# Kernel optimization log

Hardware: AMD Instinct MI355X
Metric: run time of the kernel (lower is better)

## Reference

```python
import jax, jax.numpy as jnp
import numpy as np

N_U = 50000
N_I = 50000
E = 800000
HID = 64
HEADS = 4
OUT = 32
NEG_SLOPE = 0.2


def _gat(xs, xd, e, ws, wd, a_s, a_d, b, heads, ch, n_dst, concat):
    # xs:[Ns,Fin] xd:[Nd,Fin] e:[2,E]; PyG GATConv (no self loops, eval mode)
    hs = (xs @ ws).reshape(-1, heads, ch)  # [Ns,H,C]
    hd = (xd @ wd).reshape(-1, heads, ch)  # [Nd,H,C]
    al_s = jnp.einsum('nhc,hc->nh', hs, a_s)  # [Ns,H]
    al_d = jnp.einsum('nhc,hc->nh', hd, a_d)  # [Nd,H]
    src, dst = e[0], e[1]
    alpha = jax.nn.leaky_relu(al_s[src] + al_d[dst], NEG_SLOPE)  # [E,H]
    m = jax.lax.stop_gradient(jax.ops.segment_max(alpha, dst, num_segments=n_dst))
    ealpha = jnp.exp(alpha - m[dst])
    denom = jax.ops.segment_sum(ealpha, dst, num_segments=n_dst)
    coef = ealpha / (denom[dst] + 1e-16)  # segment softmax over incoming edges
    msg = hs[src] * coef[:, :, None]  # [E,H,C]
    out = jax.ops.segment_sum(msg, dst, num_segments=n_dst)  # [Nd,H,C]
    out = out.reshape(n_dst, heads * ch) if concat else out.mean(axis=1)
    return out + b


def _forward(x_user, x_item, e_u2i, e_i2u,
             p_user_w, p_user_b, p_item_w, p_item_b,
             l0_u2i_ws, l0_u2i_wd, l0_u2i_as, l0_u2i_ad, l0_u2i_b,
             l0_i2u_ws, l0_i2u_wd, l0_i2u_as, l0_i2u_ad, l0_i2u_b,
             l1_u2i_ws, l1_u2i_wd, l1_u2i_as, l1_u2i_ad, l1_u2i_b,
             l1_i2u_ws, l1_i2u_wd, l1_i2u_as, l1_i2u_ad, l1_i2u_b):
    hu = jax.nn.elu(x_user @ p_user_w + p_user_b)
    hi = jax.nn.elu(x_item @ p_item_w + p_item_b)
    # layer 0: heads=4, concat=True, out dim HID*HEADS; HeteroConv sum (one edge type per dst)
    hi1 = _gat(hu, hi, e_u2i, l0_u2i_ws, l0_u2i_wd, l0_u2i_as, l0_u2i_ad, l0_u2i_b, HEADS, HID, N_I, True)
    hu1 = _gat(hi, hu, e_i2u, l0_i2u_ws, l0_i2u_wd, l0_i2u_as, l0_i2u_ad, l0_i2u_b, HEADS, HID, N_U, True)
    hu1 = jax.nn.elu(hu1)  # dropout is identity in eval mode
    hi1 = jax.nn.elu(hi1)
    # layer 1: heads=1, concat=False -> mean over heads
    hi2 = _gat(hu1, hi1, e_u2i, l1_u2i_ws, l1_u2i_wd, l1_u2i_as, l1_u2i_ad, l1_u2i_b, 1, OUT, N_I, False)
    hu2 = _gat(hi1, hu1, e_i2u, l1_i2u_ws, l1_i2u_wd, l1_i2u_as, l1_i2u_ad, l1_i2u_b, 1, OUT, N_U, False)
    return hu2, hi2


def setup_inputs() -> dict:
    key = jax.random.key(0)
    ks = jax.random.split(key, 32)
    s = 0.1
    d = {
        'x_user': jax.random.normal(ks[0], (N_U, 128), jnp.float32),
        'x_item': jax.random.normal(ks[1], (N_I, 128), jnp.float32),
        'e_u2i': jax.random.randint(ks[2], (2, E), 0, 50000, jnp.int32),
        'e_i2u': jax.random.randint(ks[3], (2, E), 0, 50000, jnp.int32),
        'p_user_w': jax.random.normal(ks[4], (128, HID), jnp.float32) * s,
        'p_user_b': jax.random.normal(ks[5], (HID,), jnp.float32) * s,
        'p_item_w': jax.random.normal(ks[6], (128, HID), jnp.float32) * s,
        'p_item_b': jax.random.normal(ks[7], (HID,), jnp.float32) * s,
    }
    i = 8
    for lname, fin, h, c in (('l0', HID, HEADS, HID), ('l1', HID * HEADS, 1, OUT)):
        for et in ('u2i', 'i2u'):
            odim = h * c if lname == 'l0' else c
            d[f'{lname}_{et}_ws'] = jax.random.normal(ks[i], (fin, h * c), jnp.float32) * s; i += 1
            d[f'{lname}_{et}_wd'] = jax.random.normal(ks[i], (fin, h * c), jnp.float32) * s; i += 1
            d[f'{lname}_{et}_as'] = jax.random.normal(ks[i], (h, c), jnp.float32) * s; i += 1
            d[f'{lname}_{et}_ad'] = jax.random.normal(ks[i], (h, c), jnp.float32) * s; i += 1
            d[f'{lname}_{et}_b'] = jax.random.normal(ks[i], (odim,), jnp.float32) * s; i += 1
    return d


def reference(x_user, x_item, e_u2i, e_i2u,
              p_user_w, p_user_b, p_item_w, p_item_b,
              l0_u2i_ws, l0_u2i_wd, l0_u2i_as, l0_u2i_ad, l0_u2i_b,
              l0_i2u_ws, l0_i2u_wd, l0_i2u_as, l0_i2u_ad, l0_i2u_b,
              l1_u2i_ws, l1_u2i_wd, l1_u2i_as, l1_u2i_ad, l1_u2i_b,
              l1_i2u_ws, l1_i2u_wd, l1_i2u_as, l1_i2u_ad, l1_i2u_b):
    return _forward(x_user, x_item, e_u2i, e_i2u,
                    p_user_w, p_user_b, p_item_w, p_item_b,
                    l0_u2i_ws, l0_u2i_wd, l0_u2i_as, l0_u2i_ad, l0_u2i_b,
                    l0_i2u_ws, l0_i2u_wd, l0_i2u_as, l0_i2u_ad, l0_i2u_b,
                    l1_u2i_ws, l1_u2i_wd, l1_u2i_as, l1_u2i_ad, l1_u2i_b,
                    l1_i2u_ws, l1_i2u_wd, l1_i2u_as, l1_i2u_ad, l1_i2u_b)
```

## Files before the change

### kernel.cpp

```cpp
#include <hip/hip_runtime.h>
#include <cstdint>
#include <cstddef>

#define NN 50000
#define NE 800000
#define GB 196
#define TILE1 4096
#define CAP 8192

typedef __attribute__((ext_vector_type(8))) short short8;
typedef __attribute__((ext_vector_type(4))) float floatx4;

__device__ __forceinline__ float lrelu_f(float x){ return x >= 0.f ? x : 0.2f*x; }
__device__ __forceinline__ float elu_f(float x){ return x > 0.f ? x : __expf(x) - 1.f; }

__device__ __forceinline__ unsigned short f2bf(float f){
  unsigned int u = __float_as_uint(f);
  u += 0x7FFFu + ((u >> 16) & 1u);
  return (unsigned short)(u >> 16);
}
__device__ __forceinline__ float bf2f(unsigned int us){
  return __uint_as_float(us << 16);
}
__device__ __forceinline__ float4 bf4_load(const unsigned short* p){
  uint2 q = *(const uint2*)p;
  return make_float4(bf2f(q.x & 0xffffu), bf2f(q.x >> 16),
                     bf2f(q.y & 0xffffu), bf2f(q.y >> 16));
}
__device__ __forceinline__ uint2 bf4_pack(float4 o){
  uint2 p;
  p.x = (unsigned)f2bf(o.x) | ((unsigned)f2bf(o.y) << 16);
  p.y = (unsigned)f2bf(o.z) | ((unsigned)f2bf(o.w) << 16);
  return p;
}
__device__ __forceinline__ void split_bf(float a, unsigned short& h, unsigned short& l){
  h = f2bf(a);
  l = f2bf(a - bf2f(h));
}

__device__ __forceinline__ float dot2bf(float acc, unsigned a, unsigned b){
  asm("v_dot2_f32_bf16 %0, %1, %2, %0" : "+v"(acc) : "v"(a), "v"(b));
  return acc;
}

__device__ __forceinline__ void agg_pair(float (&acc)[4][8], float (&den)[4],
                                         uint4 q0, uint4 q1, uint2 w0, uint2 w1){
  const unsigned ONE2 = 0x3F803F80u;
  unsigned wp[4];
  wp[0] = __builtin_amdgcn_perm(w1.x, w0.x, 0x05040100u);
  wp[1] = __builtin_amdgcn_perm(w1.x, w0.x, 0x07060302u);
  wp[2] = __builtin_amdgcn_perm(w1.y, w0.y, 0x05040100u);
  wp[3] = __builtin_amdgcn_perm(w1.y, w0.y, 0x07060302u);
  unsigned xp[8];
  xp[0] = __builtin_amdgcn_perm(q1.x, q0.x, 0x05040100u);
  xp[1] = __builtin_amdgcn_perm(q1.x, q0.x, 0x07060302u);
  xp[2] = __builtin_amdgcn_perm(q1.y, q0.y, 0x05040100u);
  xp[3] = __builtin_amdgcn_perm(q1.y, q0.y, 0x07060302u);
  xp[4] = __builtin_amdgcn_perm(q1.z, q0.z, 0x05040100u);
  xp[5] = __builtin_amdgcn_perm(q1.z, q0.z, 0x07060302u);
  xp[6] = __builtin_amdgcn_perm(q1.w, q0.w, 0x05040100u);
  xp[7] = __builtin_amdgcn_perm(q1.w, q0.w, 0x07060302u);
  #pragma unroll
  for (int h=0;h<4;h++){
    den[h] = dot2bf(den[h], wp[h], ONE2);
    #pragma unroll
    for (int c=0;c<8;c++) acc[h][c] = dot2bf(acc[h][c], wp[h], xp[c]);
  }
}

__global__ __launch_bounds__(256) void ghist_kernel(const int* __restrict__ e0,
                                                    const int* __restrict__ e1,
                                                    int* __restrict__ ghist){
  const int ty = blockIdx.y;
  const int* e = ty ? e1 : e0;
  __shared__ int h[GB];
  for (int j=threadIdx.x; j<GB; j+=256) h[j]=0;
  __syncthreads();
  for (int i = blockIdx.x*256 + threadIdx.x; i < NE; i += 256*256)
    atomicAdd(&h[e[NE+i]>>8], 1);
  __syncthreads();
  for (int j=threadIdx.x; j<GB; j+=256) if (h[j]) atomicAdd(&ghist[ty*200+j], h[j]);
}

__global__ __launch_bounds__(256) void gscan_kernel(const int* __restrict__ ghist,
                                                    int* __restrict__ gbase,
                                                    int* __restrict__ gcur){
  __shared__ int wb[4];
  const int t = threadIdx.x, wv = t>>6, l = t&63;
  for (int ty=0; ty<2; ++ty){
    int v = (t < GB) ? ghist[ty*200+t] : 0;
    int sum = v;
    #pragma unroll
    for (int off=1; off<64; off<<=1){
      int x = __shfl_up(sum, off, 64);
      if (l >= off) sum += x;
    }
    if (l == 63) wb[wv] = sum;
    __syncthreads();
    int wbase = 0;
    #pragma unroll
    for (int w=0; w<4; ++w) if (w < wv) wbase += wb[w];
    int excl = wbase + sum - v;
    if (t <= GB) gbase[ty*200+t] = excl;
    if (t <  GB) gcur [ty*200+t] = excl;
    __syncthreads();
  }
}

__global__ __launch_bounds__(256) void part1_kernel(const int* __restrict__ e0,
                                                    const int* __restrict__ e1,
                                                    int* __restrict__ gcur,
                                                    int2* __restrict__ p0,
                                                    int2* __restrict__ p1){
  const int ty = blockIdx.y;
  const int* e = ty ? e1 : e0;
  int2* pairs = ty ? p1 : p0;
  __shared__ int cnt[256];
  __shared__ int lstart[256];
  __shared__ int lcur[256];
  __shared__ int curg[GB];
  __shared__ int lsrc[TILE1];
  __shared__ int ldst[TILE1];
  __shared__ int wb[4];
  const int t = threadIdx.x;
  cnt[t] = 0;
  __syncthreads();
  int dreg[16], sreg[16];
  const int base = blockIdx.x*TILE1;
  const int ntile = min(TILE1, NE - base);
  #pragma unroll
  for (int it=0; it<16; ++it){
    int i = base + it*256 + t;
    int d = -1, s = 0;
    if (i < NE){ d = e[NE+i]; s = e[i]; atomicAdd(&cnt[d>>8], 1); }
    dreg[it] = d; sreg[it] = s;
  }
  __syncthreads();
  int c = cnt[t], sum = c;
  #pragma unroll
  for (int off=1; off<64; off<<=1){
    int x = __shfl_up(sum, off, 64);
    if ((t&63) >= off) sum += x;
  }
  if ((t&63) == 63) wb[t>>6] = sum;
  __syncthreads();
  int wbase = 0;
  #pragma unroll
  for (int w=0; w<4; ++w) if (w < (t>>6)) wbase += wb[w];
  int excl = wbase + sum - c;
  lstart[t] = excl;
  lcur[t] = excl;
  if (t < GB && c > 0) curg[t] = atomicAdd(&gcur[ty*200+t], c);
  __syncthreads();
  #pragma unroll
  for (int it=0; it<16; ++it){
    int d = dreg[it];
    if (d >= 0){
      int pos = atomicAdd(&lcur[d>>8], 1);
      lsrc[pos] = sreg[it];
      ldst[pos] = d;
    }
  }
  __syncthreads();
  for (int i=t; i<ntile; i+=256){
    int d = ldst[i];
    int j = d>>8;
    pairs[curg[j] + (i - lstart[j])] = make_int2(lsrc[i], d);
  }
}

struct Part2Job {
  const int2* pairs; const int* gbase;
  const float* als; const float* ald;
  int* ssrc; int* offs; unsigned short* coef;
};
__global__ __launch_bounds__(256) void part2_kernel(Part2Job j0, Part2Job j1){
  const Part2Job jb = blockIdx.y ? j1 : j0;
  const int b = blockIdx.x;
  const int t = threadIdx.x;
  __shared__ int lcnt[256];
  __shared__ int lcur[256];
  __shared__ int wb[4];
  __shared__ int sorted_src[CAP];
  __shared__ unsigned char sorted_dl[CAP];
  const int gb0 = jb.gbase[b], gb1 = jb.gbase[b+1];
  const int n = gb1 - gb0;
  lcnt[t] = 0;
  __syncthreads();
  for (int i=t; i<n; i+=256)
    atomicAdd(&lcnt[jb.pairs[gb0+i].y - (b<<8)], 1);
  __syncthreads();
  int c = lcnt[t], sum = c;
  #pragma unroll
  for (int off=1; off<64; off<<=1){
    int x = __shfl_up(sum, off, 64);
    if ((t&63) >= off) sum += x;
  }
  if ((t&63) == 63) wb[t>>6] = sum;
  __syncthreads();
  int wbase = 0;
  #pragma unroll
  for (int w=0; w<4; ++w) if (w < (t>>6)) wbase += wb[w];
  int excl = wbase + sum - c;
  lcur[t] = excl;
  int g = (b<<8) + t;
  if (g <= NN) jb.offs[g] = gb0 + excl;
  __syncthreads();
  for (int i=t; i<n; i+=256){
    int2 pr = jb.pairs[gb0+i];
    int dl = pr.y - (b<<8);
    int pos = atomicAdd(&lcur[dl], 1);
    sorted_src[pos] = pr.x;
    sorted_dl[pos] = (unsigned char)dl;
  }
  __syncthreads();
  const float4* als4 = (const float4*)jb.als;
  const float4* ald4 = (const float4*)jb.ald;
  for (int i=t; i<n; i+=256){
    int s  = sorted_src[i];
    int dl = sorted_dl[i];
    float4 a  = als4[s];
    float4 ad = ald4[(b<<8)+dl];
    float4 w;
    w.x = __expf(lrelu_f(a.x+ad.x));
    w.y = __expf(lrelu_f(a.y+ad.y));
    w.z = __expf(lrelu_f(a.z+ad.z));
    w.w = __expf(lrelu_f(a.w+ad.w));
    ((uint2*)jb.coef)[gb0+i] = bf4_pack(w);
    jb.ssrc[gb0+i] = s;
  }
}

struct WcvJob {
  const float* W; const float* cwS; const float* cwD;
  unsigned short* Wth; unsigned short* Wtl;
  int K; int N; int mode;
};
struct WcvArgs { WcvJob j[6]; };
__global__ __launch_bounds__(256) void wconv_kernel(WcvArgs args){
  WcvJob jb = args.j[blockIdx.y];
  int idx = blockIdx.x*256 + threadIdx.x;
  if (idx >= jb.K * jb.N) return;
  int k = idx / jb.N, n = idx % jb.N;
  float val;
  if (jb.mode == 0) val = jb.W[(size_t)k*jb.N + n];
  else {
    if (n < 32)       val = jb.W[(size_t)k*32 + n];
    else if (n == 32) val = jb.cwS[k];
    else if (n == 33) val = jb.cwD[k];
    else              val = 0.f;
  }
  unsigned short h, g;
  split_bf(val, h, g);
  jb.Wth[(size_t)n*jb.K + k] = h;
  jb.Wtl[(size_t)n*jb.K + k] = g;
}

struct MgJob {
  const void* A;
  const unsigned short* Wth;
  const unsigned short* Wtl;
  const float* bias;
  void* C; float* outA; float* outB;
  const float* cwS; const float* cwD;
};
template<int NT, int KK, bool ELU, bool BF16OUT, bool BF16A, bool LG, bool LOGIT>
__global__ __launch_bounds__(256) void mgemm_kernel(MgJob j0, MgJob j1,
                                                    int M, int N)
{
  const MgJob jb = blockIdx.z ? j1 : j0;
  constexpr int TN = NT*16;
  __shared__ __align__(16) unsigned short Ah[64*72];
  __shared__ __align__(16) unsigned short Al[BF16A ? 8 : 64*72];
  __shared__ __align__(16) unsigned short Bh[TN*72];
  __shared__ __align__(16) unsigned short Bl[TN*72];
  __shared__ float CwS[LOGIT ? 256 : 1];
  __shared__ float CwD[LOGIT ? 256 : 1];
  const int t = threadIdx.x;
  const int m0 = blockIdx.x*64;
  const int n0 = blockIdx.y*TN;
  const int wv = t>>6, l = t&63;
  const int lr = l&15, lq = l>>4;
  if constexpr (LOGIT){ CwS[t] = jb.cwS[t]; CwD[t] = jb.cwD[t]; }
  floatx4 acc[NT];
  #pragma unroll
  for (int i=0;i<NT;i++) acc[i] = (floatx4){0.f,0.f,0.f,0.f};

  #pragma unroll
  for (int kt=0; kt<KK; kt+=64){
    if constexpr (BF16A){
      const unsigned short* A = (const unsigned short*)jb.A;
      #pragma unroll
      for (int i=0;i<2;i++){
        int li = t + i*256;
        int r = li >> 3, c8 = (li & 7)*8;
        short8 v = {0,0,0,0,0,0,0,0};
        if (m0 + r < M) v = *(const short8*)(A + (size_t)(m0+r)*KK + kt + c8);
        *(short8*)&Ah[r*72 + c8] = v;
      }
    } else {
      const float* A = (const float*)jb.A;
      #pragma unroll
      for (int i=0;i<4;i++){
        int li = t + i*256;
        int r = li >> 4, c4 = (li & 15)*4;
        float4 v = make_float4(0.f,0.f,0.f,0.f);
        if (m0 + r < M) v = *(const float4*)(A + (size_t)(m0+r)*KK + kt + c4);
        unsigned short h0,h1,h2,h3,g0,g1,g2,g3;
        split_bf(v.x,h0,g0); split_bf(v.y,h1,g1);
        split_bf(v.z,h2,g2); split_bf(v.w,h3,g3);
        uint2 ph = { (unsigned)h0 | ((unsigned)h1<<16), (unsigned)h2 | ((unsigned)h3<<16) };
        uint2 pl = { (unsigned)g0 | ((unsigned)g1<<16), (unsigned)g2 | ((unsigned)g3<<16) };
        *(uint2*)&Ah[r*72 + c4] = ph;
        *(uint2*)&Al[r*72 + c4] = pl;
      }
    }
    for (int c = t; c < TN*8; c += 256){
      int n  = c >> 3;
      int k8 = (c & 7) * 8;
      *(short8*)&Bh[n*72 + k8] =
          *(const short8*)(jb.Wth + (size_t)(n0 + n)*KK + kt + k8);
      *(short8*)&Bl[n*72 + k8] =
          *(const short8*)(jb.Wtl + (size_t)(n0 + n)*KK + kt + k8);
    }
    __syncthreads();
    #pragma unroll
    for (int ks=0; ks<2; ks++){
      const int koff = ks*32 + lq*8;
      short8 a_h = *(const short8*)&Ah[(wv*16+lr)*72 + koff];
      short8 a_l;
      if constexpr (!BF16A) a_l = *(const short8*)&Al[(wv*16+lr)*72 + koff];
      #pragma unroll
      for (int nt=0; nt<NT; nt++){
        short8 b_h = *(const short8*)&Bh[(nt*16+lr)*72 + koff];
        short8 b_l = *(const short8*)&Bl[(nt*16+lr)*72 + koff];
        acc[nt] = __builtin_amdgcn_mfma_f32_16x16x32_bf16(a_h, b_h, acc[nt], 0,0,0);
        acc[nt] = __builtin_amdgcn_mfma_f32_16x16x32_bf16(a_h, b_l, acc[nt], 0,0,0);
        if constexpr (!BF16A)
          acc[nt] = __builtin_amdgcn_mfma_f32_16x16x32_bf16(a_l, b_h, acc[nt], 0,0,0);
      }
    }
    __syncthreads();
  }
  float ls[LOGIT ? 4 : 1][LOGIT ? 4 : 1];
  float ld_[LOGIT ? 4 : 1][LOGIT ? 4 : 1];
  if constexpr (LOGIT){
    #pragma unroll
    for (int r=0;r<4;r++)
      #pragma unroll
      for (int h=0;h<4;h++){ ls[r][h]=0.f; ld_[r][h]=0.f; }
  }
  #pragma unroll
  for (int nt=0; nt<NT; nt++){
    int n = n0 + nt*16 + lr;
    float bv = jb.bias ? jb.bias[n] : 0.f;
    #pragma unroll
    for (int r=0;r<4;r++){
      int m = m0 + wv*16 + lq*4 + r;
      if (m < M){
        float o = acc[nt][r] + bv;
        if (ELU) o = elu_f(o);
        if constexpr (LG){
          if (n < 32)       ((unsigned short*)jb.C)[(size_t)m*32 + n] = f2bf(o);
          else if (n == 32) jb.outA[m] = o;
          else if (n == 33) jb.outB[m] = o;
        } else {
          if (BF16OUT) ((unsigned short*)jb.C)[(size_t)m*N + n] = f2bf(o);
          else         ((float*)jb.C)[(size_t)m*N + n] = o;
        }
        if constexpr (LOGIT){
          #pragma unroll
          for (int h=0;h<4;h++){
            ls[r][h]  = fmaf(o, CwS[h*64 + n], ls[r][h]);
            ld_[r][h] = fmaf(o, CwD[h*64 + n], ld_[r][h]);
          }
        }
      }
    }
  }
  if constexpr (LOGIT){
    #pragma unroll
    for (int r=0;r<4;r++)
      #pragma unroll
      for (int h=0;h<4;h++){
        float a = ls[r][h], d = ld_[r][h];
        #pragma unroll
        for (int off=1; off<16; off<<=1){
          a += __shfl_xor(a, off, 64);
          d += __shfl_xor(d, off, 64);
        }
        ls[r][h]=a; ld_[r][h]=d;
      }
    if (lr == 0){
      #pragma unroll
      for (int r=0;r<4;r++){
        int m = m0 + wv*16 + lq*4 + r;
        if (m < M){
          #pragma unroll
          for (int h=0;h<4;h++){
            jb.outA[(size_t)m*4 + h] = ls[r][h];
            jb.outB[(size_t)m*4 + h] = ld_[r][h];
          }
        }
      }
    }
  }
}

struct HgJob {
  const unsigned short* A;
  const unsigned short* Wth;
  const unsigned short* Wtl;
  const float* den;
  const float* bias; unsigned short* out;
};
__global__ __launch_bounds__(256) void hgemm_kernel(HgJob j0, HgJob j1){
  const HgJob jb = blockIdx.z ? j1 : j0;
  const int head = blockIdx.y;
  const int m0 = blockIdx.x*64;
  __shared__ __align__(16) unsigned short Ah[64*72];
  __shared__ __align__(16) unsigned short Bh[64*72];
  __shared__ __align__(16) unsigned short Bl[64*72];
  const int t = threadIdx.x;
  const int wv = t>>6, l = t&63;
  const int lr = l&15, lq = l>>4;
  floatx4 acc[4];
  #pragma unroll
  for (int i=0;i<4;i++) acc[i] = (floatx4){0.f,0.f,0.f,0.f};
  #pragma unroll
  for (int i=0;i<2;i++){
    int li = t + i*256;
    int r = li >> 3, c8 = (li & 7)*8;
    short8 v = {0,0,0,0,0,0,0,0};
    if (m0 + r < NN) v = *(const short8*)(jb.A + (size_t)(m0+r)*256 + head*64 + c8);
    *(short8*)&Ah[r*72 + c8] = v;
  }
  #pragma unroll
  for (int i=0;i<2;i++){
    int c  = t + i*256;
    int n  = c >> 3;
    int k8 = (c & 7) * 8;
    *(short8*)&Bh[n*72 + k8] =
        *(const short8*)(jb.Wth + (size_t)(head*64 + n)*64 + k8);
    *(short8*)&Bl[n*72 + k8] =
        *(const short8*)(jb.Wtl + (size_t)(head*64 + n)*64 + k8);
  }
  __syncthreads();
  #pragma unroll
  for (int ks=0; ks<2; ks++){
    const int koff = ks*32 + lq*8;
    short8 a_h = *(const short8*)&Ah[(wv*16+lr)*72 + koff];
    #pragma unroll
    for (int nt=0; nt<4; nt++){
      short8 b_h = *(const short8*)&Bh[(nt*16+lr)*72 + koff];
      short8 b_l = *(const short8*)&Bl[(nt*16+lr)*72 + koff];
      acc[nt] = __builtin_amdgcn_mfma_f32_16x16x32_bf16(a_h, b_h, acc[nt], 0,0,0);
      acc[nt] = __builtin_amdgcn_mfma_f32_16x16x32_bf16(a_h, b_l, acc[nt], 0,0,0);
    }
  }
  float inv[4];
  #pragma unroll
  for (int r=0;r<4;r++){
    int m = m0 + wv*16 + lq*4 + r;
    inv[r] = (m < NN) ? 1.f/(jb.den[(size_t)m*4 + head] + 1e-16f) : 0.f;
  }
  #pragma unroll
  for (int nt=0; nt<4; nt++){
    int col = head*64 + nt*16 + lr;
    float bv = jb.bias[col];
    #pragma unroll
    for (int r=0;r<4;r++){
      int m = m0 + wv*16 + lq*4 + r;
      if (m < NN)
        jb.out[(size_t)m*256 + col] = f2bf(elu_f(acc[nt][r]*inv[r] + bv));
    }
  }
}

struct CollapseJob { const float* W; const float* a; float* out; int K,H,C; };
struct CollapseArgs { CollapseJob j[8]; };
__global__ void collapse_kernel(CollapseArgs args){
  CollapseJob jb = args.j[blockIdx.x];
  int t = threadIdx.x;
  if (t < jb.K * jb.H){
    int k = t / jb.H, h = t % jb.H;
    const float* wr = jb.W + (size_t)k * (jb.H*jb.C) + h*jb.C;
    const float* ar = jb.a + h*jb.C;
    float s = 0.f;
    for (int c=0;c<jb.C;c++) s += wr[c]*ar[c];
    jb.out[h*jb.K + k] = s;
  }
}

struct AggPJob {
  const int* offs; const int* ssrc;
  const unsigned short* x;
  const unsigned short* coef;
  unsigned short* agg;
  float* den;
};
__global__ __launch_bounds__(256) void aggpre_kernel(AggPJob ja, AggPJob jbb){
  const AggPJob jb = blockIdx.y ? jbb : ja;
  const int tid = threadIdx.x;
  const int lane = tid & 63, wid = tid >> 6;
  const int grp = lane >> 3;
  const int cl  = lane & 7;
  const int c8  = cl * 8;
  const int dst = blockIdx.x*32 + wid*8 + grp;
  if (dst >= NN) return;
  const int b0 = jb.offs[dst], b1 = jb.offs[dst+1];
  float acc[4][8];
  float den[4] = {0.f,0.f,0.f,0.f};
  #pragma unroll
  for (int h=0;h<4;h++)
    #pragma unroll
    for (int c=0;c<8;c++) acc[h][c]=0.f;
  int e = b0;
  for (; e+3 < b1; e += 4){
    int s0 = jb.ssrc[e];
    int s1 = jb.ssrc[e+1];
    int s2 = jb.ssrc[e+2];
    int s3 = jb.ssrc[e+3];
    uint4 q0 = *(const uint4*)(jb.x + ((size_t)s0<<6) + c8);
    uint4 q1 = *(const uint4*)(jb.x + ((size_t)s1<<6) + c8);
    uint4 q2 = *(const uint4*)(jb.x + ((size_t)s2<<6) + c8);
    uint4 q3 = *(const uint4*)(jb.x + ((size_t)s3<<6) + c8);
    uint2 w0 = *(const uint2*)(jb.coef + (size_t)e*4);
    uint2 w1 = *(const uint2*)(jb.coef + (size_t)(e+1)*4);
    uint2 w2 = *(const uint2*)(jb.coef + (size_t)(e+2)*4);
    uint2 w3 = *(const uint2*)(jb.coef + (size_t)(e+3)*4);
    agg_pair(acc, den, q0, q1, w0, w1);
    agg_pair(acc, den, q2, q3, w2, w3);
  }
  if (e+1 < b1){
    int s0 = jb.ssrc[e];
    int s1 = jb.ssrc[e+1];
    uint4 q0 = *(const uint4*)(jb.x + ((size_t)s0<<6) + c8);
    uint4 q1 = *(const uint4*)(jb.x + ((size_t)s1<<6) + c8);
    uint2 w0 = *(const uint2*)(jb.coef + (size_t)e*4);
    uint2 w1 = *(const uint2*)(jb.coef + (size_t)(e+1)*4);
    agg_pair(acc, den, q0, q1, w0, w1);
    e += 2;
  }
  if (e < b1){
    int s = jb.ssrc[e];
    uint4 q = *(const uint4*)(jb.x + ((size_t)s<<6) + c8);
    uint2 w = *(const uint2*)(jb.coef + (size_t)e*4);
    float wf[4] = { bf2f(w.x & 0xffffu), bf2f(w.x >> 16),
                    bf2f(w.y & 0xffffu), bf2f(w.y >> 16) };
    float xf[8] = { bf2f(q.x & 0xffffu), bf2f(q.x >> 16),
                    bf2f(q.y & 0xffffu), bf2f(q.y >> 16),
                    bf2f(q.z & 0xffffu), bf2f(q.z >> 16),
                    bf2f(q.w & 0xffffu), bf2f(q.w >> 16) };
    #pragma unroll
    for (int h=0;h<4;h++){
      den[h] += wf[h];
      #pragma unroll
      for (int c=0;c<8;c++) acc[h][c] += wf[h]*xf[c];
    }
  }
  #pragma unroll
  for (int h=0;h<4;h++){
    uint2 plo = bf4_pack(make_float4(acc[h][0],acc[h][1],acc[h][2],acc[h][3]));
    uint2 phi = bf4_pack(make_float4(acc[h][4],acc[h][5],acc[h][6],acc[h][7]));
    uint4 pk = { plo.x, plo.y, phi.x, phi.y };
    *(uint4*)(jb.agg + (size_t)dst*256 + h*64 + c8) = pk;
  }
  if (cl == 0)
    *(float4*)(jb.den + (size_t)dst*4) = make_float4(den[0],den[1],den[2],den[3]);
}

struct Agg1Job {
  const int* offs; const int* ssrc;
  const unsigned short* hs;
  const float* als; const float* ald;
  const float* bias; float* out;
};
__global__ __launch_bounds__(256) void agg1_kernel(Agg1Job ja, Agg1Job jbb){
  const Agg1Job jb = blockIdx.y ? jbb : ja;
  const int tid = threadIdx.x;
  const int lane = tid & 63, wid = tid >> 6;
  const int grp = lane >> 3;
  const int cl  = lane & 7;
  const int c4  = cl * 4;
  const int dst = blockIdx.x*32 + wid*8 + grp;
  if (dst >= NN) return;
  const int b0 = jb.offs[dst], b1 = jb.offs[dst+1];
  const float ad = jb.ald[dst];
  float acc[4] = {0.f,0.f,0.f,0.f};
  float den = 0.f;
  int e = b0;
  for (; e+3 < b1; e += 4){
    int s0 = jb.ssrc[e];
    int s1 = jb.ssrc[e+1];
    int s2 = jb.ssrc[e+2];
    int s3 = jb.ssrc[e+3];
    float a0 = jb.als[s0];
    float a1 = jb.als[s1];
    float a2 = jb.als[s2];
    float a3 = jb.als[s3];
    float4 v0 = bf4_load(jb.hs + ((size_t)s0<<5) + c4);
    float4 v1 = bf4_load(jb.hs + ((size_t)s1<<5) + c4);
    float4 v2 = bf4_load(jb.hs + ((size_t)s2<<5) + c4);
    float4 v3 = bf4_load(jb.hs + ((size_t)s3<<5) + c4);
    float w0 = __expf(lrelu_f(a0 + ad));
    float w1 = __expf(lrelu_f(a1 + ad));
    float w2 = __expf(lrelu_f(a2 + ad));
    float w3 = __expf(lrelu_f(a3 + ad));
    acc[0] += w0*v0.x + w1*v1.x + w2*v2.x + w3*v3.x;
    acc[1] += w0*v0.y + w1*v1.y + w2*v2.y + w3*v3.y;
    acc[2] += w0*v0.z + w1*v1.z + w2*v2.z + w3*v3.z;
    acc[3] += w0*v0.w + w1*v1.w + w2*v2.w + w3*v3.w;
    den += (w0 + w1) + (w2 + w3);
  }
  for (; e < b1; ++e){
    int s = jb.ssrc[e];
    float w = __expf(lrelu_f(jb.als[s] + ad));
    float4 v = bf4_load(jb.hs + ((size_t)s<<5) + c4);
    acc[0] += w*v.x; acc[1] += w*v.y; acc[2] += w*v.z; acc[3] += w*v.w;
    den += w;
  }
  const float inv = 1.f/(den + 1e-16f);
  float4 b = *(const float4*)(jb.bias + c4);
  float4 o = make_float4(acc[0]*inv+b.x, acc[1]*inv+b.y,
                         acc[2]*inv+b.z, acc[3]*inv+b.w);
  *(float4*)(jb.out + (size_t)dst*32 + c4) = o;
}

extern "C" void kernel_launch(void* const* d_in, const int* in_sizes, int n_in,
                              void* d_out, int out_size, void* d_ws, size_t ws_size,
                              hipStream_t stream)
{
  (void)in_sizes; (void)n_in; (void)out_size; (void)ws_size;
  const float* x_user   = (const float*)d_in[0];
  const float* x_item   = (const float*)d_in[1];
  const int*   e_u2i    = (const int*)  d_in[2];
  const int*   e_i2u    = (const int*)  d_in[3];
  const float* p_user_w = (const float*)d_in[4];
  const float* p_user_b = (const float*)d_in[5];
  const float* p_item_w = (const float*)d_in[6];
  const float* p_item_b = (const float*)d_in[7];
  const float* l0_u2i_ws=(const float*)d_in[8];
  const float* l0_u2i_wd=(const float*)d_in[9];
  const float* l0_u2i_as=(const float*)d_in[10];
  const float* l0_u2i_ad=(const float*)d_in[11];
  const float* l0_u2i_b =(const float*)d_in[12];
  const float* l0_i2u_ws=(const float*)d_in[13];
  const float* l0_i2u_wd=(const float*)d_in[14];
  const float* l0_i2u_as=(const float*)d_in[15];
  const float* l0_i2u_ad=(const float*)d_in[16];
  const float* l0_i2u_b =(const float*)d_in[17];
  const float* l1_u2i_ws=(const float*)d_in[18];
  const float* l1_u2i_wd=(const float*)d_in[19];
  const float* l1_u2i_as=(const float*)d_in[20];
  const float* l1_u2i_ad=(const float*)d_in[21];
  const float* l1_u2i_b =(const float*)d_in[22];
  const float* l1_i2u_ws=(const float*)d_in[23];
  const float* l1_i2u_wd=(const float*)d_in[24];
  const float* l1_i2u_as=(const float*)d_in[25];
  const float* l1_i2u_ad=(const float*)d_in[26];
  const float* l1_i2u_b =(const float*)d_in[27];

  char* base = (char*)d_ws;
  size_t off = 0;
  auto alloc = [&](size_t bytes)->void*{
    void* p = base + off;
    off += (bytes + 255) & ~(size_t)255;
    return p;
  };
  int* offs_u2i = (int*)alloc((size_t)(NN+1)*sizeof(int));
  int* offs_i2u = (int*)alloc((size_t)(NN+1)*sizeof(int));
  int* ssrc_u2i = (int*)alloc((size_t)NE*sizeof(int));
  int* ssrc_i2u = (int*)alloc((size_t)NE*sizeof(int));
  int* ghist    = (int*)alloc((size_t)2*200*sizeof(int));
  int* gbase    = (int*)alloc((size_t)2*200*sizeof(int));
  int* gcur     = (int*)alloc((size_t)2*200*sizeof(int));
  unsigned short* coef0_u2i = (unsigned short*)alloc((size_t)NE*4*sizeof(unsigned short));
  unsigned short* coef0_i2u = (unsigned short*)alloc((size_t)NE*4*sizeof(unsigned short));
  unsigned short* hu = (unsigned short*)alloc((size_t)NN*64*sizeof(unsigned short));
  unsigned short* hi = (unsigned short*)alloc((size_t)NN*64*sizeof(unsigned short));
  unsigned short* agg_u2i = (unsigned short*)alloc((size_t)NN*256*sizeof(unsigned short));
  unsigned short* agg_i2u = (unsigned short*)alloc((size_t)NN*256*sizeof(unsigned short));
  float* den_u2i = (float*)alloc((size_t)NN*4*sizeof(float));
  float* den_i2u = (float*)alloc((size_t)NN*4*sizeof(float));
  unsigned short* hu1 = (unsigned short*)alloc((size_t)NN*256*sizeof(unsigned short));
  unsigned short* hi1 = (unsigned short*)alloc((size_t)NN*256*sizeof(unsigned short));
  unsigned short* hs1_u2i = (unsigned short*)alloc((size_t)NN*32*sizeof(unsigned short));
  unsigned short* hs1_i2u = (unsigned short*)alloc((size_t)NN*32*sizeof(unsigned short));
  float* als0_u2i = (float*)alloc((size_t)NN*4*sizeof(float));
  float* ald0_u2i = (float*)alloc((size_t)NN*4*sizeof(float));
  float* als0_i2u = (float*)alloc((size_t)NN*4*sizeof(float));
  float* ald0_i2u = (float*)alloc((size_t)NN*4*sizeof(float));
  float* als1_u2i = (float*)alloc((size_t)NN*sizeof(float));
  float* ald1_u2i = (float*)alloc((size_t)NN*sizeof(float));
  float* als1_i2u = (float*)alloc((size_t)NN*sizeof(float));
  float* ald1_i2u = (float*)alloc((size_t)NN*sizeof(float));
  float* cw0s_u2i = (float*)alloc(256*sizeof(float));
  float* cw0d_u2i = (float*)alloc(256*sizeof(float));
  float* cw0s_i2u = (float*)alloc(256*sizeof(float));
  float* cw0d_i2u = (float*)alloc(256*sizeof(float));
  float* cw1s_u2i = (float*)alloc(256*sizeof(float));
  float* cw1d_u2i = (float*)alloc(256*sizeof(float));
  float* cw1s_i2u = (float*)alloc(256*sizeof(float));
  float* cw1d_i2u = (float*)alloc(256*sizeof(float));
  unsigned short* wt_pu_h  = (unsigned short*)alloc((size_t)64*128*sizeof(unsigned short));
  unsigned short* wt_pu_l  = (unsigned short*)alloc((size_t)64*128*sizeof(unsigned short));
  unsigned short* wt_pi_h  = (unsigned short*)alloc((size_t)64*128*sizeof(unsigned short));
  unsigned short* wt_pi_l  = (unsigned short*)alloc((size_t)64*128*sizeof(unsigned short));
  unsigned short* wt_l0u_h = (unsigned short*)alloc((size_t)256*64*sizeof(unsigned short));
  unsigned short* wt_l0u_l = (unsigned short*)alloc((size_t)256*64*sizeof(unsigned short));
  unsigned short* wt_l0i_h = (unsigned short*)alloc((size_t)256*64*sizeof(unsigned short));
  unsigned short* wt_l0i_l = (unsigned short*)alloc((size_t)256*64*sizeof(unsigned short));
  unsigned short* wt_wcu_h = (unsigned short*)alloc((size_t)48*256*sizeof(unsigned short));
  unsigned short* wt_wcu_l = (unsigned short*)alloc((size_t)48*256*sizeof(unsigned short));
  unsigned short* wt_wci_h = (unsigned short*)alloc((size_t)48*256*sizeof(unsigned short));
  unsigned short* wt_wci_l = (unsigned short*)alloc((size_t)48*256*sizeof(unsigned short));
  int2* pairs_u2i = (int2*)hu1;
  int2* pairs_i2u = pairs_u2i + NE;

  const int GM = (NN + 63)/64;

  hipMemsetAsync(ghist, 0, (size_t)2*200*sizeof(int), stream);
  ghist_kernel<<<dim3(256,2), 256, 0, stream>>>(e_u2i, e_i2u, ghist);
  gscan_kernel<<<1, 256, 0, stream>>>(ghist, gbase, gcur);
  part1_kernel<<<dim3((NE+TILE1-1)/TILE1,2), 256, 0, stream>>>(
      e_u2i, e_i2u, gcur, pairs_u2i, pairs_i2u);

  CollapseArgs ca;
  ca.j[0] = {l0_u2i_ws, l0_u2i_as, cw0s_u2i, 64, 4, 64};
  ca.j[1] = {l0_u2i_wd, l0_u2i_ad, cw0d_u2i, 64, 4, 64};
  ca.j[2] = {l0_i2u_ws, l0_i2u_as, cw0s_i2u, 64, 4, 64};
  ca.j[3] = {l0_i2u_wd, l0_i2u_ad, cw0d_i2u, 64, 4, 64};
  ca.j[4] = {l1_u2i_ws, l1_u2i_as, cw1s_u2i, 256, 1, 32};
  ca.j[5] = {l1_u2i_wd, l1_u2i_ad, cw1d_u2i, 256, 1, 32};
  ca.j[6] = {l1_i2u_ws, l1_i2u_as, cw1s_i2u, 256, 1, 32};
  ca.j[7] = {l1_i2u_wd, l1_i2u_ad, cw1d_i2u, 256, 1, 32};
  collapse_kernel<<<8, 256, 0, stream>>>(ca);

  WcvArgs wa;
  wa.j[0] = {p_user_w,  nullptr,   nullptr,   wt_pu_h,  wt_pu_l,  128, 64, 0};
  wa.j[1] = {p_item_w,  nullptr,   nullptr,   wt_pi_h,  wt_pi_l,  128, 64, 0};
  wa.j[2] = {l0_u2i_ws, nullptr,   nullptr,   wt_l0u_h, wt_l0u_l, 64, 256, 0};
  wa.j[3] = {l0_i2u_ws, nullptr,   nullptr,   wt_l0i_h, wt_l0i_l, 64, 256, 0};
  wa.j[4] = {l1_u2i_ws, cw1s_u2i,  cw1d_i2u,  wt_wcu_h, wt_wcu_l, 256, 48, 1};
  wa.j[5] = {l1_i2u_ws, cw1s_i2u,  cw1d_u2i,  wt_wci_h, wt_wci_l, 256, 48, 1};
  wconv_kernel<<<dim3(64,6), 256, 0, stream>>>(wa);

  mgemm_kernel<4,128,true,true,false,false,true><<<dim3(GM,1,2), 256, 0, stream>>>(
      MgJob{x_user, wt_pu_h, wt_pu_l, p_user_b, hu, als0_u2i, ald0_i2u, cw0s_u2i, cw0d_i2u},
      MgJob{x_item, wt_pi_h, wt_pi_l, p_item_b, hi, als0_i2u, ald0_u2i, cw0s_i2u, cw0d_u2i},
      NN, 64);

  part2_kernel<<<dim3(GB,2), 256, 0, stream>>>(
      Part2Job{pairs_u2i, gbase,       als0_u2i, ald0_u2i, ssrc_u2i, offs_u2i, coef0_u2i},
      Part2Job{pairs_i2u, gbase + 200, als0_i2u, ald0_i2u, ssrc_i2u, offs_i2u, coef0_i2u});

  aggpre_kernel<<<dim3((NN+31)/32,2), 256, 0, stream>>>(
      AggPJob{offs_u2i, ssrc_u2i, hu, coef0_u2i, agg_u2i, den_u2i},
      AggPJob{offs_i2u, ssrc_i2u, hi, coef0_i2u, agg_i2u, den_i2u});

  hgemm_kernel<<<dim3(GM,4,2), 256, 0, stream>>>(
      HgJob{agg_u2i, wt_l0u_h, wt_l0u_l, den_u2i, l0_u2i_b, hi1},
      HgJob{agg_i2u, wt_l0i_h, wt_l0i_l, den_i2u, l0_i2u_b, hu1});

  mgemm_kernel<3,256,false,true,true,true,false><<<dim3(GM,1,2), 256, 0, stream>>>(
      MgJob{hu1, wt_wcu_h, wt_wcu_l, nullptr, hs1_u2i, als1_u2i, ald1_i2u, nullptr, nullptr},
      MgJob{hi1, wt_wci_h, wt_wci_l, nullptr, hs1_i2u, als1_i2u, ald1_u2i, nullptr, nullptr},
      NN, 48);

  float* hu2 = (float*)d_out;
  float* hi2 = (float*)d_out + (size_t)NN*32;
  agg1_kernel<<<dim3((NN+31)/32,2), 256, 0, stream>>>(
      Agg1Job{offs_u2i, ssrc_u2i, hs1_u2i, als1_u2i, ald1_u2i, l1_u2i_b, hi2},
      Agg1Job{offs_i2u, ssrc_i2u, hs1_i2u, als1_i2u, ald1_i2u, l1_i2u_b, hu2});
}
```

Baseline: 349.3 us.

## Fuse layer-0 output GEMM with layer-1 projection GEMM via shared-memory tile

Merges the per-head layer-0 output GEMM (normalize, bias, ELU) and the following layer-1 projection GEMM into one kernel. The 64x256 hidden tile is kept in LDS instead of being written to and re-read from global memory as hu1/hi1. This also removes one kernel launch. In exchange the grid shrinks from four head-blocks per row tile to one, each block loops over heads serially, and the larger LDS footprint may lower occupancy.

```diff
diff --git a/kernel.cpp b/kernel.cpp
--- a/kernel.cpp
+++ b/kernel.cpp
@@ -407,72 +407,121 @@
   }
 }
 
-struct HgJob {
+struct FsJob {
   const unsigned short* A;
-  const unsigned short* Wth;
-  const unsigned short* Wtl;
+  const unsigned short* W0h;
+  const unsigned short* W0l;
   const float* den;
-  const float* bias; unsigned short* out;
+  const float* b0;
+  const unsigned short* Wch;
+  const unsigned short* Wcl;
+  unsigned short* hs1;
+  float* outA; float* outB;
 };
-__global__ __launch_bounds__(256) void hgemm_kernel(HgJob j0, HgJob j1){
-  const HgJob jb = blockIdx.z ? j1 : j0;
-  const int head = blockIdx.y;
+__global__ __launch_bounds__(256) void l0l1_kernel(FsJob j0, FsJob j1, int M){
+  const FsJob jb = blockIdx.z ? j1 : j0;
+  __shared__ __align__(16) unsigned short H1[64*264];
+  __shared__ __align__(16) unsigned short Sa[64*72];
+  __shared__ __align__(16) unsigned short Sbh[64*72];
+  __shared__ __align__(16) unsigned short Sbl[64*72];
+  const int t = threadIdx.x;
   const int m0 = blockIdx.x*64;
-  __shared__ __align__(16) unsigned short Ah[64*72];
-  __shared__ __align__(16) unsigned short Bh[64*72];
-  __shared__ __align__(16) unsigned short Bl[64*72];
-  const int t = threadIdx.x;
   const int wv = t>>6, l = t&63;
   const int lr = l&15, lq = l>>4;
-  floatx4 acc[4];
-  #pragma unroll
-  for (int i=0;i<4;i++) acc[i] = (floatx4){0.f,0.f,0.f,0.f};
-  #pragma unroll
-  for (int i=0;i<2;i++){
-    int li = t + i*256;
-    int r = li >> 3, c8 = (li & 7)*8;
-    short8 v = {0,0,0,0,0,0,0,0};
-    if (m0 + r < NN) v = *(const short8*)(jb.A + (size_t)(m0+r)*256 + head*64 + c8);
-    *(short8*)&Ah[r*72 + c8] = v;
-  }
-  #pragma unroll
-  for (int i=0;i<2;i++){
-    int c  = t + i*256;
-    int n  = c >> 3;
-    int k8 = (c & 7) * 8;
-    *(short8*)&Bh[n*72 + k8] =
-        *(const short8*)(jb.Wth + (size_t)(head*64 + n)*64 + k8);
-    *(short8*)&Bl[n*72 + k8] =
-        *(const short8*)(jb.Wtl + (size_t)(head*64 + n)*64 + k8);
-  }
-  __syncthreads();
-  #pragma unroll
-  for (int ks=0; ks<2; ks++){
-    const int koff = ks*32 + lq*8;
-    short8 a_h = *(const short8*)&Ah[(wv*16+lr)*72 + koff];
-    #pragma unroll
-    for (int nt=0; nt<4; nt++){
-      short8 b_h = *(const short8*)&Bh[(nt*16+lr)*72 + koff];
-      short8 b_l = *(const short8*)&Bl[(nt*16+lr)*72 + koff];
-      acc[nt] = __builtin_amdgcn_mfma_f32_16x16x32_bf16(a_h, b_h, acc[nt], 0,0,0);
-      acc[nt] = __builtin_amdgcn_mfma_f32_16x16x32_bf16(a_h, b_l, acc[nt], 0,0,0);
-    }
-  }
-  float inv[4];
-  #pragma unroll
-  for (int r=0;r<4;r++){
-    int m = m0 + wv*16 + lq*4 + r;
-    inv[r] = (m < NN) ? 1.f/(jb.den[(size_t)m*4 + head] + 1e-16f) : 0.f;
-  }
-  #pragma unroll
-  for (int nt=0; nt<4; nt++){
-    int col = head*64 + nt*16 + lr;
-    float bv = jb.bias[col];
+
+  for (int h=0; h<4; ++h){
+    #pragma unroll
+    for (int i=0;i<2;i++){
+      int li = t + i*256;
+      int r = li >> 3, c8 = (li & 7)*8;
+      short8 v = {0,0,0,0,0,0,0,0};
+      if (m0 + r < M) v = *(const short8*)(jb.A + (size_t)(m0+r)*256 + h*64 + c8);
+      *(short8*)&Sa[r*72 + c8] = v;
+    }
+    #pragma unroll
+    for (int i=0;i<2;i++){
+      int c  = t + i*256;
+      int n  = c >> 3;
+      int k8 = (c & 7) * 8;
+      *(short8*)&Sbh[n*72 + k8] =
+          *(const short8*)(jb.W0h + (size_t)(h*64 + n)*64 + k8);
+      *(short8*)&Sbl[n*72 + k8] =
+          *(const short8*)(jb.W0l + (size_t)(h*64 + n)*64 + k8);
+    }
+    __syncthreads();
+    floatx4 acc[4];
+    #pragma unroll
+    for (int i=0;i<4;i++) acc[i] = (floatx4){0.f,0.f,0.f,0.f};
+    #pragma unroll
+    for (int ks=0; ks<2; ks++){
+      const int koff = ks*32 + lq*8;
+      short8 a_h = *(const short8*)&Sa[(wv*16+lr)*72 + koff];
+      #pragma unroll
+      for (int nt=0; nt<4; nt++){
+        short8 b_h = *(const short8*)&Sbh[(nt*16+lr)*72 + koff];
+        short8 b_l = *(const short8*)&Sbl[(nt*16+lr)*72 + koff];
+        acc[nt] = __builtin_amdgcn_mfma_f32_16x16x32_bf16(a_h, b_h, acc[nt], 0,0,0);
+        acc[nt] = __builtin_amdgcn_mfma_f32_16x16x32_bf16(a_h, b_l, acc[nt], 0,0,0);
+      }
+    }
+    float inv[4];
     #pragma unroll
     for (int r=0;r<4;r++){
       int m = m0 + wv*16 + lq*4 + r;
-      if (m < NN)
-        jb.out[(size_t)m*256 + col] = f2bf(elu_f(acc[nt][r]*inv[r] + bv));
+      inv[r] = (m < M) ? 1.f/(jb.den[(size_t)m*4 + h] + 1e-16f) : 0.f;
+    }
+    #pragma unroll
+    for (int nt=0; nt<4; nt++){
+      int col = h*64 + nt*16 + lr;
+      float bv = jb.b0[col];
+      #pragma unroll
+      for (int r=0;r<4;r++){
+        int mrow = wv*16 + lq*4 + r;
+        H1[mrow*264 + col] = f2bf(elu_f(acc[nt][r]*inv[r] + bv));
+      }
+    }
+    __syncthreads();
+  }
+
+  floatx4 acc2[3];
+  #pragma unroll
+  for (int i=0;i<3;i++) acc2[i] = (floatx4){0.f,0.f,0.f,0.f};
+  for (int kt=0; kt<4; ++kt){
+    for (int c = t; c < 48*8; c += 256){
+      int n  = c >> 3;
+      int k8 = (c & 7) * 8;
+      *(short8*)&Sbh[n*72 + k8] =
+          *(const short8*)(jb.Wch + (size_t)n*256 + kt*64 + k8);
+      *(short8*)&Sbl[n*72 + k8] =
+          *(const short8*)(jb.Wcl + (size_t)n*256 + kt*64 + k8);
+    }
+    __syncthreads();
+    #pragma unroll
+    for (int ks=0; ks<2; ks++){
+      const int koff = ks*32 + lq*8;
+      short8 a_h = *(const short8*)&H1[(wv*16+lr)*264 + kt*64 + koff];
+      #pragma unroll
+      for (int nt=0; nt<3; nt++){
+        short8 b_h = *(const short8*)&Sbh[(nt*16+lr)*72 + koff];
+        short8 b_l = *(const short8*)&Sbl[(nt*16+lr)*72 + koff];
+        acc2[nt] = __builtin_amdgcn_mfma_f32_16x16x32_bf16(a_h, b_h, acc2[nt], 0,0,0);
+        acc2[nt] = __builtin_amdgcn_mfma_f32_16x16x32_bf16(a_h, b_l, acc2[nt], 0,0,0);
+      }
+    }
+    __syncthreads();
+  }
+  #pragma unroll
+  for (int nt=0; nt<3; nt++){
+    int n = nt*16 + lr;
+    #pragma unroll
+    for (int r=0;r<4;r++){
+      int m = m0 + wv*16 + lq*4 + r;
+      if (m < M){
+        float o = acc2[nt][r];
+        if (n < 32)       jb.hs1[(size_t)m*32 + n] = f2bf(o);
+        else if (n == 32) jb.outA[m] = o;
+        else if (n == 33) jb.outB[m] = o;
+      }
     }
   }
 }
@@ -759,14 +808,12 @@
       AggPJob{offs_u2i, ssrc_u2i, hu, coef0_u2i, agg_u2i, den_u2i},
       AggPJob{offs_i2u, ssrc_i2u, hi, coef0_i2u, agg_i2u, den_i2u});
 
-  hgemm_kernel<<<dim3(GM,4,2), 256, 0, stream>>>(
-      HgJob{agg_u2i, wt_l0u_h, wt_l0u_l, den_u2i, l0_u2i_b, hi1},
-      HgJob{agg_i2u, wt_l0i_h, wt_l0i_l, den_i2u, l0_i2u_b, hu1});
-
-  mgemm_kernel<3,256,false,true,true,true,false><<<dim3(GM,1,2), 256, 0, stream>>>(
-      MgJob{hu1, wt_wcu_h, wt_wcu_l, nullptr, hs1_u2i, als1_u2i, ald1_i2u, nullptr, nullptr},
-      MgJob{hi1, wt_wci_h, wt_wci_l, nullptr, hs1_i2u, als1_i2u, ald1_u2i, nullptr, nullptr},
-      NN, 48);
+  l0l1_kernel<<<dim3(GM,1,2), 256, 0, stream>>>(
+      FsJob{agg_i2u, wt_l0i_h, wt_l0i_l, den_i2u, l0_i2u_b,
+            wt_wcu_h, wt_wcu_l, hs1_u2i, als1_u2i, ald1_i2u},
+      FsJob{agg_u2i, wt_l0u_h, wt_l0u_l, den_u2i, l0_u2i_b,
+            wt_wci_h, wt_wci_l, hs1_i2u, als1_i2u, ald1_u2i},
+      NN);
 
   float* hu2 = (float*)d_out;
   float* hi2 = (float*)d_out + (size_t)NN*32;
```

Measured after the change: 348.8 us. About the same (-0.1%).
